# Performance work log

Hardware: AMD Instinct MI355X
Metric: run time of the kernel (lower is better)

## Reference

```python
import jax, jax.numpy as jnp
import numpy as np


def setup_inputs() -> dict:
    key = jax.random.key(0)
    k1, k2, k3 = jax.random.split(key, 3)
    B, CIN, T, K = 64, 64, 1, 4096
    COUT, F = 64, 4
    L = F * K  # 16384; gather index space per (b, o)
    x = jax.random.normal(k1, (B, CIN, T, K), dtype=jnp.float32)
    upsample_params = jax.random.normal(k2, (CIN, COUT, F), dtype=jnp.float32)
    indices = jax.random.randint(k3, (L,), 0, L, dtype=jnp.int64 if jax.config.jax_enable_x64 else jnp.int32)
    return {"x": x, "upsample_params": upsample_params, "indices": indices}


def reference(x, upsample_params, indices):
    # x: [B, Cin, T, K]; params: [Cin, Cout, 4] -> res: [B, Cout, 4, K]
    res = jnp.einsum('bitk,iof->bofk', x, upsample_params)
    B, O = res.shape[0], res.shape[1]
    L = indices.shape[0]  # == 4*K
    # torch: flatten + index_select with per-(b,o) offset == gather along last axis
    flat = res.reshape(B, O, L)
    out = jnp.take(flat, indices, axis=2)
    return out.reshape(B, O, 1, L)
```

## Files before the change

kernel.cpp:

```cpp
#include <hip/hip_runtime.h>


typedef __attribute__((ext_vector_type(8))) short short8;
typedef __attribute__((ext_vector_type(4))) float floatx4;

#define NB    64
#define CIN   64
#define COUT  64
#define KDIM  4096
#define LDIM  16384
#define ITERS 8
#define BXS2  72
#define XT_BYTES ((size_t)NB * KDIM * CIN * 2)

__device__ __forceinline__ unsigned short f2bf(float f) {
  union { float f; unsigned u; } v; v.f = f;
  unsigned r = v.u + 0x7FFFu + ((v.u >> 16) & 1u);
  return (unsigned short)(r >> 16);
}

__global__ __launch_bounds__(256) void transpose_bf16(const float* __restrict__ x,
                                                      unsigned short* __restrict__ xt) {
  __shared__ float tile[64 * 65];
  const int t = threadIdx.x;
  const int b = blockIdx.y;
  const int k0 = blockIdx.x * 64;
  const float4* x4 = (const float4*)x;
#pragma unroll
  for (int p = 0; p < 4; ++p) {
    int i  = p * 16 + (t >> 4);
    int kq = t & 15;
    float4 v = x4[(size_t)(b * CIN + i) * (KDIM / 4) + (k0 >> 2) + kq];
    tile[i * 65 + kq * 4 + 0] = v.x;
    tile[i * 65 + kq * 4 + 1] = v.y;
    tile[i * 65 + kq * 4 + 2] = v.z;
    tile[i * 65 + kq * 4 + 3] = v.w;
  }
  __syncthreads();
  unsigned int* xt32 = (unsigned int*)xt;
  const int ip = (t & 31) * 2;
#pragma unroll
  for (int p = 0; p < 8; ++p) {
    int k = p * 8 + (t >> 5);
    unsigned lo = f2bf(tile[ip * 65 + k]);
    unsigned hi = f2bf(tile[(ip + 1) * 65 + k]);
    xt32[((size_t)b * KDIM + k0 + k) * (CIN / 2) + (ip >> 1)] = lo | (hi << 16);
  }
}

__global__ __launch_bounds__(256) void prepack_afrag(const float* __restrict__ p,
                                                     unsigned short* __restrict__ pb) {
  const int t = blockIdx.x * 256 + threadIdx.x;
  const int lane = t & 63;
  const int mk = t >> 6;
  const int mt = mk >> 3, kt = mk & 7;
  const int o = mt * 16 + (lane & 15);
  const int quad = lane >> 4;
#pragma unroll
  for (int j = 0; j < 8; ++j) {
    int s = kt * 32 + quad * 8 + j;
    int i = s & 63, g = s >> 6;
    pb[t * 8 + j] = f2bf(p[(i * COUT + o) * 4 + g]);
  }
}

__global__ __launch_bounds__(256, 4) void gemm_lds2(const unsigned short* __restrict__ xt,
                                                    const unsigned short* __restrict__ pb,
                                                    const int* __restrict__ idx,
                                                    float* __restrict__ out) {
  __shared__ __align__(16) unsigned short Bx2[64 * BXS2];
  __shared__ int fpv[64];

  const int t = threadIdx.x;
  const int b = blockIdx.y;
  const int w = t >> 6;
  const int lane = t & 63;
  const int lane15 = lane & 15;
  const int quad = lane >> 4;

  short8 af[8];
  {
    const short8* pbv = (const short8*)pb;
#pragma unroll
    for (int kt = 0; kt < 8; ++kt)
      af[kt] = pbv[(w * 8 + kt) * 64 + lane];
  }

  const unsigned short* xb = xt + (size_t)b * KDIM * CIN;
  const int u = t & 3;
  const int lrow = t >> 2;

  uint4 d0, d1; int fp;
  {
    const int l_base = blockIdx.x * (ITERS * 64);
    const int iv = idx[l_base + lrow];
    const uint4* xrow = (const uint4*)(xb + (size_t)(iv & (KDIM - 1)) * CIN);
    d0 = xrow[2 * u];
    d1 = xrow[2 * u + 1];
    fp = iv >> 12;
  }

  const short8 z8 = {0, 0, 0, 0, 0, 0, 0, 0};

  for (int it = 0; it < ITERS; ++it) {
    __syncthreads();
    *(uint4*)&Bx2[lrow * BXS2 + u * 16]     = d0;
    *(uint4*)&Bx2[lrow * BXS2 + u * 16 + 8] = d1;
    if (u == 0) fpv[lrow] = fp;
    __syncthreads();

    if (it + 1 < ITERS) {
      const int l_base = (blockIdx.x * ITERS + it + 1) * 64;
      const int iv = idx[l_base + lrow];
      const uint4* xrow = (const uint4*)(xb + (size_t)(iv & (KDIM - 1)) * CIN);
      d0 = xrow[2 * u];
      d1 = xrow[2 * u + 1];
      fp = iv >> 12;
    }

    floatx4 acc[4] = {floatx4{0.f, 0.f, 0.f, 0.f}, floatx4{0.f, 0.f, 0.f, 0.f},
                      floatx4{0.f, 0.f, 0.f, 0.f}, floatx4{0.f, 0.f, 0.f, 0.f}};
#pragma unroll
    for (int nt = 0; nt < 4; ++nt) {
      const int lr = nt * 16 + lane15;
      const short8 ev = *(const short8*)&Bx2[lr * BXS2 + quad * 8];
      const short8 ov = *(const short8*)&Bx2[lr * BXS2 + 32 + quad * 8];
      const int fpl = fpv[lr];
#pragma unroll
      for (int kt = 0; kt < 8; ++kt) {
        const short8 h  = (kt & 1) ? ov : ev;
        const short8 bf = (fpl == (kt >> 1)) ? h : z8;
        acc[nt] = __builtin_amdgcn_mfma_f32_16x16x32_bf16(af[kt], bf, acc[nt], 0, 0, 0);
      }
    }

    const int l_base = (blockIdx.x * ITERS + it) * 64;
#pragma unroll
    for (int nt = 0; nt < 4; ++nt) {
      const int l = l_base + nt * 16 + lane15;
#pragma unroll
      for (int r = 0; r < 4; ++r) {
        const int o = w * 16 + quad * 4 + r;
        out[((size_t)(b * COUT + o)) * LDIM + l] = acc[nt][r];
      }
    }
  }
}

extern "C" void kernel_launch(void* const* d_in, const int* in_sizes, int n_in,
                              void* d_out, int out_size, void* d_ws, size_t ws_size,
                              hipStream_t stream) {
  const float* x      = (const float*)d_in[0];
  const float* params = (const float*)d_in[1];
  const int*   idx    = (const int*)d_in[2];
  float* out = (float*)d_out;
  unsigned short* xt = (unsigned short*)d_ws;
  unsigned short* pb = (unsigned short*)((char*)d_ws + XT_BYTES);

  transpose_bf16<<<dim3(KDIM / 64, NB), 256, 0, stream>>>(x, xt);
  prepack_afrag<<<dim3(8), 256, 0, stream>>>(params, pb);
  gemm_lds2<<<dim3(LDIM / (64 * ITERS), NB), 256, 0, stream>>>(xt, pb, idx, out);
}
```

Before: 348.2 us.

## Double-buffer gather LDS tile, prefetch indices two ahead, use nontemporal stores

The gather kernel now keeps two LDS buffers, which lets it drop one of the two barriers per iteration. It also prefetches the index for iteration it+2 so the dependent row load no longer waits on an index load. Output writes switch to nontemporal stores to reduce cache pollution from the large streaming output. The costs are more LDS per block and reliance on a hand-placed waitcnt and barrier for correctness.

```diff
diff --git a/kernel.cpp b/kernel.cpp
--- a/kernel.cpp
+++ b/kernel.cpp
@@ -64,12 +64,12 @@
   }
 }
 
-__global__ __launch_bounds__(256, 4) void gemm_lds2(const unsigned short* __restrict__ xt,
-                                                    const unsigned short* __restrict__ pb,
-                                                    const int* __restrict__ idx,
-                                                    float* __restrict__ out) {
-  __shared__ __align__(16) unsigned short Bx2[64 * BXS2];
-  __shared__ int fpv[64];
+__global__ __launch_bounds__(256, 4) void gemm_db(const unsigned short* __restrict__ xt,
+                                                  const unsigned short* __restrict__ pb,
+                                                  const int* __restrict__ idx,
+                                                  float* __restrict__ out) {
+  __shared__ __align__(16) unsigned short Bx[2][64 * BXS2];
+  __shared__ int fpv[2][64];
 
   const int t = threadIdx.x;
   const int b = blockIdx.y;
@@ -89,33 +89,35 @@
   const unsigned short* xb = xt + (size_t)b * KDIM * CIN;
   const int u = t & 3;
   const int lrow = t >> 2;
+  const int lb0 = blockIdx.x * (ITERS * 64);
 
-  uint4 d0, d1; int fp;
+  uint4 d0, d1; int fp, ivn;
   {
-    const int l_base = blockIdx.x * (ITERS * 64);
-    const int iv = idx[l_base + lrow];
-    const uint4* xrow = (const uint4*)(xb + (size_t)(iv & (KDIM - 1)) * CIN);
-    d0 = xrow[2 * u];
-    d1 = xrow[2 * u + 1];
-    fp = iv >> 12;
+    const int iv0 = idx[lb0 + lrow];
+    const uint4* r0 = (const uint4*)(xb + (size_t)(iv0 & (KDIM - 1)) * CIN);
+    d0 = r0[2 * u];
+    d1 = r0[2 * u + 1];
+    fp = iv0 >> 12;
+    ivn = idx[lb0 + 64 + lrow];
   }
 
   const short8 z8 = {0, 0, 0, 0, 0, 0, 0, 0};
 
   for (int it = 0; it < ITERS; ++it) {
-    __syncthreads();
-    *(uint4*)&Bx2[lrow * BXS2 + u * 16]     = d0;
-    *(uint4*)&Bx2[lrow * BXS2 + u * 16 + 8] = d1;
-    if (u == 0) fpv[lrow] = fp;
-    __syncthreads();
+    const int p = it & 1;
+    *(uint4*)&Bx[p][lrow * BXS2 + u * 16]     = d0;
+    *(uint4*)&Bx[p][lrow * BXS2 + u * 16 + 8] = d1;
+    if (u == 0) fpv[p][lrow] = fp;
+    asm volatile("s_waitcnt lgkmcnt(0)" ::: "memory");
+    __builtin_amdgcn_s_barrier();
+    asm volatile("" ::: "memory");
 
     if (it + 1 < ITERS) {
-      const int l_base = (blockIdx.x * ITERS + it + 1) * 64;
-      const int iv = idx[l_base + lrow];
-      const uint4* xrow = (const uint4*)(xb + (size_t)(iv & (KDIM - 1)) * CIN);
-      d0 = xrow[2 * u];
-      d1 = xrow[2 * u + 1];
-      fp = iv >> 12;
+      fp = ivn >> 12;
+      const uint4* rn = (const uint4*)(xb + (size_t)(ivn & (KDIM - 1)) * CIN);
+      d0 = rn[2 * u];
+      d1 = rn[2 * u + 1];
+      if (it + 2 < ITERS) ivn = idx[lb0 + (it + 2) * 64 + lrow];
     }
 
     floatx4 acc[4] = {floatx4{0.f, 0.f, 0.f, 0.f}, floatx4{0.f, 0.f, 0.f, 0.f},
@@ -123,9 +125,9 @@
 #pragma unroll
     for (int nt = 0; nt < 4; ++nt) {
       const int lr = nt * 16 + lane15;
-      const short8 ev = *(const short8*)&Bx2[lr * BXS2 + quad * 8];
-      const short8 ov = *(const short8*)&Bx2[lr * BXS2 + 32 + quad * 8];
-      const int fpl = fpv[lr];
+      const short8 ev = *(const short8*)&Bx[p][lr * BXS2 + quad * 8];
+      const short8 ov = *(const short8*)&Bx[p][lr * BXS2 + 32 + quad * 8];
+      const int fpl = fpv[p][lr];
 #pragma unroll
       for (int kt = 0; kt < 8; ++kt) {
         const short8 h  = (kt & 1) ? ov : ev;
@@ -134,14 +136,14 @@
       }
     }
 
-    const int l_base = (blockIdx.x * ITERS + it) * 64;
+    const int l_base = lb0 + it * 64;
 #pragma unroll
     for (int nt = 0; nt < 4; ++nt) {
       const int l = l_base + nt * 16 + lane15;
 #pragma unroll
       for (int r = 0; r < 4; ++r) {
         const int o = w * 16 + quad * 4 + r;
-        out[((size_t)(b * COUT + o)) * LDIM + l] = acc[nt][r];
+        __builtin_nontemporal_store(acc[nt][r], &out[((size_t)(b * COUT + o)) * LDIM + l]);
       }
     }
   }
@@ -159,5 +161,5 @@
 
   transpose_bf16<<<dim3(KDIM / 64, NB), 256, 0, stream>>>(x, xt);
   prepack_afrag<<<dim3(8), 256, 0, stream>>>(params, pb);
-  gemm_lds2<<<dim3(LDIM / (64 * ITERS), NB), 256, 0, stream>>>(xt, pb, idx, out);
+  gemm_db<<<dim3(LDIM / (64 * ITERS), NB), 256, 0, stream>>>(xt, pb, idx, out);
 }
```

Measured after the change: 348.0 us. No clear change (-0.1%).
